# Kernel tuning notes

Hardware: AMD Instinct MI355X
Metric: run time of the kernel (lower is better)

The kernel has to match this reference:

```python
import jax, jax.numpy as jnp
import numpy as np

HIDDEN = 3072
HEADS = 32
HEAD_DIM = HIDDEN // HEADS  # 96


def setup_inputs() -> dict:
    key = jax.random.key(0)
    k1, k2, k3, k4 = jax.random.split(key, 4)
    B, S = 2, 2048
    x = jax.random.normal(k1, (B, S, HIDDEN), dtype=jnp.float32)
    # qkv_proj: Linear(hidden, 3*hidden, bias=False); torch weight is [out,in]
    w_qkv = jax.random.normal(k2, (3 * HIDDEN, HIDDEN), dtype=jnp.float32) * (HIDDEN ** -0.5)
    # o_proj: Linear(hidden, hidden) with bias
    w_o = jax.random.normal(k3, (HIDDEN, HIDDEN), dtype=jnp.float32) * (HIDDEN ** -0.5)
    b_o = jax.random.normal(k4, (HIDDEN,), dtype=jnp.float32) * 0.01
    return {"x": x, "w_qkv": w_qkv, "w_o": w_o, "b_o": b_o}


def reference(x, w_qkv, w_o, b_o):
    B, S, _ = x.shape
    qkv = jnp.einsum('bsh,oh->bso', x, w_qkv)  # [B,S,3*HIDDEN]
    q, k, v = jnp.split(qkv, 3, axis=-1)
    # [B,S,HIDDEN] -> [B,H,S,D]
    def split_heads(t):
        return t.reshape(B, S, HEADS, HEAD_DIM).transpose(0, 2, 1, 3)
    q, k, v = split_heads(q), split_heads(k), split_heads(v)
    scores = jnp.einsum('bhqd,bhkd->bhqk', q, k) / jnp.sqrt(jnp.float32(HEAD_DIM))
    attn = jax.nn.softmax(scores, axis=-1)
    out = jnp.einsum('bhqk,bhkd->bhqd', attn, v)  # [B,H,S,D]
    out = out.transpose(0, 2, 1, 3).reshape(B, S, HIDDEN)
    return jnp.einsum('bsh,oh->bso', out, w_o) + b_o
```

## Files before the change

kernel.cpp:

```cpp
#include <hip/hip_runtime.h>
#include <math.h>


typedef unsigned int u32;
typedef unsigned short u16;
typedef __attribute__((ext_vector_type(8))) short bf16x8;
typedef __attribute__((ext_vector_type(4))) float f32x4;

#define MFMA(a, b, c) __builtin_amdgcn_mfma_f32_16x16x32_bf16((a), (b), (c), 0, 0, 0)

#define GLDS16(g, l) __builtin_amdgcn_global_load_lds( \
    (const __attribute__((address_space(1))) u32*)(g), \
    (__attribute__((address_space(3))) u32*)(l), 16, 0, 0)

__device__ __forceinline__ u16 f2bf(float f) {
  u32 u = __builtin_bit_cast(u32, f);
  return (u16)((u + 0x7fffu + ((u >> 16) & 1u)) >> 16);
}
__device__ __forceinline__ float bf2f(u16 h) {
  u32 u = ((u32)h) << 16;
  return __builtin_bit_cast(float, u);
}
__device__ __forceinline__ void split2(float f, u16& h, u16& l) {
  h = f2bf(f);
  l = f2bf(f - bf2f(h));
}
__device__ __forceinline__ bf16x8 ld16(const u16* p) {
  return *reinterpret_cast<const bf16x8*>(p);
}

__global__ void split_kernel(const float* __restrict__ src, u16* __restrict__ dst,
                             long n) {
  long i = ((long)blockIdx.x * 256 + threadIdx.x) * 4;
  if (i >= n) return;
  const float4 v = *reinterpret_cast<const float4*>(src + i);
  const u32 i32 = (u32)i;
  const u32 row = i32 / 3072u;
  const u32 col = i32 - row * 3072u;
  const long base = (long)row * 6144 + (col >> 5) * 64 + (col & 31);
  ushort4 h, l;
  split2(v.x, h.x, l.x);
  split2(v.y, h.y, l.y);
  split2(v.z, h.z, l.z);
  split2(v.w, h.w, l.w);
  *reinterpret_cast<ushort4*>(dst + base) = h;
  *reinterpret_cast<ushort4*>(dst + base + 32) = l;
}

template <int MODE>
__global__ __launch_bounds__(512, 2) void gemm3t(
    const u16* __restrict__ A2, const u16* __restrict__ B2,
    int M, int N,
    u16* __restrict__ C2, float* __restrict__ Cf, const float* __restrict__ bias) {
  constexpr int NT = 96;
  __shared__ u16 ldsA[2][256 * 64];
  __shared__ u16 ldsB[2][192 * 64];
  const int tid = threadIdx.x;
  const int lane = tid & 63;
  const int w = tid >> 6;
  const int wr = w >> 2, wc = w & 3;
  const int lr = lane & 15, lg = lane >> 4;

  const int mt = M >> 8;
  const int nwg = gridDim.x;
  const int bid = blockIdx.x;
  const int wg = (bid & 7) * (nwg >> 3) + (bid >> 3);
  const int bm = wg % mt, bn = wg / mt;

  const int srow = lane >> 3;
  const int sgc = ((lane & 7) ^ srow) * 8;

  auto stA = [&](int buf, int kt, int j) {
    const int r = j * 64 + w * 8 + srow;
    GLDS16(A2 + (long)(bm * 256 + r) * 6144 + kt * 64 + sgc,
           &ldsA[buf][(j * 64 + w * 8) * 64]);
  };
  auto stB = [&](int buf, int kt, int j) {
    const int r = j * 64 + w * 8 + srow;
    GLDS16(B2 + (long)(bn * 192 + r) * 6144 + kt * 64 + sgc,
           &ldsB[buf][(j * 64 + w * 8) * 64]);
  };

  f32x4 acc[8][3];
#pragma unroll
  for (int m = 0; m < 8; ++m)
#pragma unroll
    for (int n = 0; n < 3; ++n)
#pragma unroll
      for (int j = 0; j < 4; ++j) acc[m][n][j] = 0.f;

  stA(0, 0, 0); stA(0, 0, 1); stA(0, 0, 2); stA(0, 0, 3);
  stB(0, 0, 0); stB(0, 0, 1); stB(0, 0, 2);
  asm volatile("s_waitcnt vmcnt(0)" ::: "memory");
  __builtin_amdgcn_s_barrier();

  const int aRow0 = wr * 128 + lr;
  const int bRow0 = wc * 48 + lr;
  const int c0 = (lg ^ (lr & 7)) * 8;

#define RD_A(MQ)                                                           \
  _Pragma("unroll") for (int m = 0; m < 4; ++m) {                          \
    const int off = (aRow0 + (MQ)*64 + m * 16) * 64 + c0;                  \
    ah[m] = ld16(&LA[off]);                                                \
    al[m] = ld16(&LA[off ^ 32]);                                           \
  }
#define DO_MFMA3(MQ)                                                       \
  __builtin_amdgcn_s_setprio(1);                                           \
  _Pragma("unroll") for (int m = 0; m < 4; ++m)                            \
  _Pragma("unroll") for (int n = 0; n < 3; ++n) {                          \
    acc[(MQ)*4 + m][n] = MFMA(ah[m], bh[n], acc[(MQ)*4 + m][n]);           \
    acc[(MQ)*4 + m][n] = MFMA(ah[m], bl[n], acc[(MQ)*4 + m][n]);           \
    acc[(MQ)*4 + m][n] = MFMA(al[m], bh[n], acc[(MQ)*4 + m][n]);           \
  }                                                                        \
  __builtin_amdgcn_s_setprio(0);
#define PH_SYNC()                                                          \
  __builtin_amdgcn_s_barrier();                                            \
  asm volatile("s_waitcnt lgkmcnt(0)" ::: "memory");                       \
  __builtin_amdgcn_sched_barrier(0);

  for (int t = 0; t < NT; ++t) {
    const int cur = t & 1;
    const int nxt = cur ^ 1;
    const u16* LA = ldsA[cur];
    const u16* LB = ldsB[cur];
    bf16x8 ah[4], al[4], bh[3], bl[3];
#pragma unroll
    for (int n = 0; n < 3; ++n) {
      const int off = (bRow0 + n * 16) * 64 + c0;
      bh[n] = ld16(&LB[off]);
      bl[n] = ld16(&LB[off ^ 32]);
    }
    RD_A(0);
    if (t + 1 < NT) {
      stA(nxt, t + 1, 0); stA(nxt, t + 1, 1);
      stA(nxt, t + 1, 2); stA(nxt, t + 1, 3);
      stB(nxt, t + 1, 0); stB(nxt, t + 1, 1); stB(nxt, t + 1, 2);
    }
    PH_SYNC();
    DO_MFMA3(0);
    __builtin_amdgcn_s_barrier();
    RD_A(1);
    PH_SYNC();
    DO_MFMA3(1);
    asm volatile("s_waitcnt vmcnt(0)" ::: "memory");
    __builtin_amdgcn_s_barrier();
  }
#undef RD_A
#undef DO_MFMA3
#undef PH_SYNC

#pragma unroll
  for (int m = 0; m < 8; ++m)
#pragma unroll
    for (int j = 0; j < 4; ++j) {
      const long row = (long)bm * 256 + wr * 128 + m * 16 + lg * 4 + j;
#pragma unroll
      for (int n = 0; n < 3; ++n) {
        const int col = bn * 192 + wc * 48 + n * 16 + lr;
        const float v = acc[m][n][j];
        if (MODE == 0) {
          const long idx = row * (2L * N) + (col >> 5) * 64 + (col & 31);
          u16 h, l;
          split2(v, h, l);
          C2[idx] = h;
          C2[idx + 32] = l;
        } else {
          Cf[row * N + col] = v + bias[col];
        }
      }
    }
}

__global__ void pack_k(const u16* __restrict__ QKV2, u16* __restrict__ Kp) {
  const int t = blockIdx.x * 256 + threadIdx.x;
  const int lane = t & 63;
  const int rec3 = t >> 6;
  const int c = rec3 % 3;
  const int kb = (rec3 / 3) & 127;
  const int hl = rec3 / 384;
  const int lr = lane & 15, lg = lane >> 4;
  const long src = ((long)((hl >> 5) * 2048 + kb * 16 + lr)) * 18432 +
                   (96 + (hl & 31) * 3 + c) * 64 + lg * 8;
  const long dst = ((long)rec3 * 2) * 512 + lane * 8;
  *reinterpret_cast<bf16x8*>(Kp + dst) = ld16(QKV2 + src);
  *reinterpret_cast<bf16x8*>(Kp + dst + 512) = ld16(QKV2 + src + 32);
}

__global__ __launch_bounds__(256) void pack_v(const u16* __restrict__ QKV2,
                                              u16* __restrict__ Vp) {
  __shared__ u16 sV[2][32 * 96];
  const int tid = threadIdx.x;
  const int hl = blockIdx.x >> 6;
  const int kq = blockIdx.x & 63;
  const long rowbase = ((long)((hl >> 5) * 2048 + kq * 32)) * 18432 +
                       (192 + (hl & 31) * 3) * 64;
#pragma unroll
  for (int i = 0; i < 3; ++i) {
    const int idx = i * 256 + tid;
    const int pl = idx / 384;
    const int r2 = idx % 384;
    const int row = r2 / 12, cu = r2 % 12;
    const long src = rowbase + (long)row * 18432 + (cu >> 2) * 64 + (cu & 3) * 8 + pl * 32;
    *reinterpret_cast<bf16x8*>(&sV[pl][row * 96 + cu * 8]) = ld16(QKV2 + src);
  }
  __syncthreads();
#pragma unroll
  for (int i = 0; i < 3; ++i) {
    const int idx = i * 256 + tid;
    const int lane = idx & 63;
    const int rl = idx >> 6;
    const int n = rl >> 1, pl = rl & 1;
    const int lr = lane & 15, lg = lane >> 4;
    bf16x8 o;
#pragma unroll
    for (int e = 0; e < 8; ++e) o[e] = (short)sV[pl][(lg * 8 + e) * 96 + n * 16 + lr];
    const long dst = ((((long)hl * 6 + n) * 64 + kq) * 2 + pl) * 512 + lane * 8;
    *reinterpret_cast<bf16x8*>(Vp + dst) = o;
  }
}

__global__ __launch_bounds__(256, 2) void attn_kernel(
    const u16* __restrict__ QKV2,
    const u16* __restrict__ Kp, const u16* __restrict__ Vp,
    u16* __restrict__ AO2) {
  __shared__ u16 kv[2][24 * 512];
  __shared__ u16 pb[4][2][512];
  const int lane = threadIdx.x & 63;
  const int wv = threadIdx.x >> 6;
  const int lr = lane & 15, lg = lane >> 4;

  const int nwg = gridDim.x;
  const int bid = blockIdx.x;
  const int wg = (bid & 7) * (nwg >> 3) + (bid >> 3);
  const int hl = wg >> 5;
  const int qblk = wg & 31;
  const int b = hl >> 5;
  const int q0 = qblk * 64 + wv * 16;

  bf16x8 qh[3], ql[3];
  {
    const long qofs =
        ((long)(b * 2048 + q0 + lr)) * 18432 + ((hl & 31) * 3) * 64 + lg * 8;
#pragma unroll
    for (int c = 0; c < 3; ++c) {
      qh[c] = ld16(QKV2 + qofs + c * 64);
      ql[c] = ld16(QKV2 + qofs + c * 64 + 32);
    }
  }

  f32x4 o_acc[6];
#pragma unroll
  for (int n = 0; n < 6; ++n)
#pragma unroll
    for (int j = 0; j < 4; ++j) o_acc[n][j] = 0.f;
  float lsum[4] = {0.f, 0.f, 0.f, 0.f};

  const float scale = 0.10206207261596577f;
  u16* pbh = pb[wv][0];
  u16* pbl = pb[wv][1];

  auto stage = [&](int nb, int it) {
    const long kbase = ((long)hl * 768 + (long)it * 12) * 512;
    const long vbase = ((long)hl * 768 + (long)it * 2) * 512;
#pragma unroll
    for (int j = 0; j < 6; ++j) {
      const int r = wv * 6 + j;
      const u16* src;
      if (r < 12) {
        const int tt = r / 6, rc = r % 6;
        src = Kp + kbase + ((long)(tt * 6 + rc)) * 512 + lane * 8;
      } else {
        const int r2 = r - 12;
        src = Vp + vbase + ((long)((r2 >> 1) * 128 + (r2 & 1))) * 512 + lane * 8;
      }
      GLDS16(src, &kv[nb][r * 512]);
    }
  };

  stage(0, 0);
  __syncthreads();

  for (int it = 0; it < 64; ++it) {
    const int nb = it & 1;
    if (it < 63) stage(nb ^ 1, it + 1);
    const u16* L = kv[nb];

    f32x4 s0, s1;
#pragma unroll
    for (int j = 0; j < 4; ++j) { s0[j] = 0.f; s1[j] = 0.f; }
#pragma unroll
    for (int c = 0; c < 3; ++c) {
      const bf16x8 kh0 = ld16(L + (c * 2 + 0) * 512 + lane * 8);
      const bf16x8 kl0 = ld16(L + (c * 2 + 1) * 512 + lane * 8);
      const bf16x8 kh1 = ld16(L + (6 + c * 2 + 0) * 512 + lane * 8);
      const bf16x8 kl1 = ld16(L + (6 + c * 2 + 1) * 512 + lane * 8);
      s0 = MFMA(qh[c], kh0, s0);
      s1 = MFMA(qh[c], kh1, s1);
      s0 = MFMA(qh[c], kl0, s0);
      s1 = MFMA(qh[c], kl1, s1);
      s0 = MFMA(ql[c], kh0, s0);
      s1 = MFMA(ql[c], kh1, s1);
    }

#pragma unroll
    for (int j = 0; j < 4; ++j) {
      const float p0 = __expf(fmaf(s0[j], scale, -12.f));
      const float p1 = __expf(fmaf(s1[j], scale, -12.f));
      lsum[j] += p0 + p1;
      const int r = lg * 4 + j;
      const int key = j ^ lg;
      u16 h, l;
      split2(p0, h, l);
      const int a0 = r * 32 + ((((lr >> 3) ^ key) & 3) << 3) + (lr & 7);
      pbh[a0] = h;
      pbl[a0] = l;
      split2(p1, h, l);
      const int a1 = r * 32 + ((((2 + (lr >> 3)) ^ key) & 3) << 3) + (lr & 7);
      pbh[a1] = h;
      pbl[a1] = l;
    }
    const int rkey = (lr & 3) ^ (lr >> 2);
    const int ra = lr * 32 + (((lg ^ rkey) & 3) << 3);
    const bf16x8 pah = ld16(&pbh[ra]);
    const bf16x8 pal = ld16(&pbl[ra]);

#pragma unroll
    for (int n = 0; n < 6; ++n) {
      const bf16x8 vh = ld16(L + (12 + n * 2 + 0) * 512 + lane * 8);
      const bf16x8 vl = ld16(L + (12 + n * 2 + 1) * 512 + lane * 8);
      o_acc[n] = MFMA(pah, vh, o_acc[n]);
      o_acc[n] = MFMA(pah, vl, o_acc[n]);
      o_acc[n] = MFMA(pal, vh, o_acc[n]);
    }
    __syncthreads();
  }

  float inv[4];
#pragma unroll
  for (int j = 0; j < 4; ++j) {
    float rs = lsum[j];
#pragma unroll
    for (int mk = 1; mk < 16; mk <<= 1) rs += __shfl_xor(rs, mk);
    inv[j] = 1.f / rs;
  }
#pragma unroll
  for (int n = 0; n < 6; ++n)
#pragma unroll
    for (int j = 0; j < 4; ++j) {
      const long row = (long)(b * 2048 + q0 + lg * 4 + j);
      const long idx =
          row * 6144 + ((hl & 31) * 3 + (n >> 1)) * 64 + (n & 1) * 16 + lr;
      u16 h, l;
      split2(o_acc[n][j] * inv[j], h, l);
      AO2[idx] = h;
      AO2[idx + 32] = l;
    }
}

extern "C" void kernel_launch(void* const* d_in, const int* in_sizes, int n_in,
                              void* d_out, int out_size, void* d_ws, size_t ws_size,
                              hipStream_t stream) {
  const float* x = (const float*)d_in[0];
  const float* wqkv = (const float*)d_in[1];
  const float* wo = (const float*)d_in[2];
  const float* bo = (const float*)d_in[3];
  float* out = (float*)d_out;
  char* ws = (char*)d_ws;

  const size_t E_X = (size_t)4096 * 3072;
  const size_t E_WQ = (size_t)9216 * 3072;
  const size_t E_QKV = (size_t)4096 * 9216;
  const size_t E_WO = (size_t)3072 * 3072;

  u16* X2 = (u16*)ws;
  char* W0 = ws + 4 * E_X;
  u16* W2 = (u16*)W0;
  char* Q0 = W0 + 4 * E_WQ;
  u16* QKV2 = (u16*)Q0;
  char* V0 = Q0 + 4 * E_QKV;
  u16* VP = (u16*)V0;
  u16* KP = (u16*)ws;
  u16* AO2 = (u16*)W0;
  u16* WO2 = (u16*)(W0 + 4 * E_X);

  const size_t need = 4 * (E_X + E_WQ + E_QKV + E_X);
  if (ws_size < need) return;

  split_kernel<<<12288, 256, 0, stream>>>(x, X2, (long)E_X);
  split_kernel<<<27648, 256, 0, stream>>>(wqkv, W2, (long)E_WQ);
  gemm3t<0><<<768, 512, 0, stream>>>(X2, W2, 4096, 9216, QKV2, nullptr, nullptr);
  pack_k<<<6144, 256, 0, stream>>>(QKV2, KP);
  pack_v<<<4096, 256, 0, stream>>>(QKV2, VP);
  split_kernel<<<9216, 256, 0, stream>>>(wo, WO2, (long)E_WO);
  attn_kernel<<<2048, 256, 0, stream>>>(QKV2, KP, VP, AO2);
  gemm3t<1><<<256, 512, 0, stream>>>(AO2, WO2, 4096, 3072, nullptr, out, bo);
}
```

Before: 1.303 ms.

## Halve GEMM workgroup to four waves with larger per-wave tiles

The split-bf16 GEMM drops from 8 waves to 4 waves per 256x192 tile. Each wave now computes a 128x96 sub-tile with 48 accumulators, and the two-phase barrier/setprio pipeline is replaced by a single load-all-then-MFMA loop with __syncthreads. The aim is to raise per-wave register reuse of A/B fragments and cut barrier count. The cost is heavy register pressure (192 accumulator VGPRs plus fragments) and less latency hiding with only 4 waves and one block per CU.

```diff
diff --git a/kernel.cpp b/kernel.cpp
--- a/kernel.cpp
+++ b/kernel.cpp
@@ -48,7 +48,7 @@
 }
 
 template <int MODE>
-__global__ __launch_bounds__(512, 2) void gemm3t(
+__global__ __launch_bounds__(256, 1) void gemm3t(
     const u16* __restrict__ A2, const u16* __restrict__ B2,
     int M, int N,
     u16* __restrict__ C2, float* __restrict__ Cf, const float* __restrict__ bias) {
@@ -58,7 +58,7 @@
   const int tid = threadIdx.x;
   const int lane = tid & 63;
   const int w = tid >> 6;
-  const int wr = w >> 2, wc = w & 3;
+  const int wr = w >> 1, wc = w & 1;
   const int lr = lane & 15, lg = lane >> 4;
 
   const int mt = M >> 8;
@@ -70,84 +70,71 @@
   const int srow = lane >> 3;
   const int sgc = ((lane & 7) ^ srow) * 8;
 
+  const u16* Apan = A2 + (size_t)(bm * 256) * 6144;
+  const u16* Bpan = B2 + (size_t)(bn * 192) * 6144;
+  const u32 laneOff = (u32)((w * 8 + srow) * 6144 + sgc);
+
   auto stA = [&](int buf, int kt, int j) {
-    const int r = j * 64 + w * 8 + srow;
-    GLDS16(A2 + (long)(bm * 256 + r) * 6144 + kt * 64 + sgc,
-           &ldsA[buf][(j * 64 + w * 8) * 64]);
+    GLDS16(Apan + (size_t)kt * 64 + (size_t)j * (32 * 6144) + laneOff,
+           &ldsA[buf][(j * 32 + w * 8) * 64]);
   };
   auto stB = [&](int buf, int kt, int j) {
-    const int r = j * 64 + w * 8 + srow;
-    GLDS16(B2 + (long)(bn * 192 + r) * 6144 + kt * 64 + sgc,
-           &ldsB[buf][(j * 64 + w * 8) * 64]);
+    GLDS16(Bpan + (size_t)kt * 64 + (size_t)j * (32 * 6144) + laneOff,
+           &ldsB[buf][(j * 32 + w * 8) * 64]);
   };
 
-  f32x4 acc[8][3];
+  f32x4 acc[8][6];
 #pragma unroll
   for (int m = 0; m < 8; ++m)
 #pragma unroll
-    for (int n = 0; n < 3; ++n)
+    for (int n = 0; n < 6; ++n)
 #pragma unroll
       for (int j = 0; j < 4; ++j) acc[m][n][j] = 0.f;
 
-  stA(0, 0, 0); stA(0, 0, 1); stA(0, 0, 2); stA(0, 0, 3);
-  stB(0, 0, 0); stB(0, 0, 1); stB(0, 0, 2);
-  asm volatile("s_waitcnt vmcnt(0)" ::: "memory");
-  __builtin_amdgcn_s_barrier();
+#pragma unroll
+  for (int j = 0; j < 8; ++j) stA(0, 0, j);
+#pragma unroll
+  for (int j = 0; j < 6; ++j) stB(0, 0, j);
+  __syncthreads();
 
   const int aRow0 = wr * 128 + lr;
-  const int bRow0 = wc * 48 + lr;
+  const int bRow0 = wc * 96 + lr;
   const int c0 = (lg ^ (lr & 7)) * 8;
-
-#define RD_A(MQ)                                                           \
-  _Pragma("unroll") for (int m = 0; m < 4; ++m) {                          \
-    const int off = (aRow0 + (MQ)*64 + m * 16) * 64 + c0;                  \
-    ah[m] = ld16(&LA[off]);                                                \
-    al[m] = ld16(&LA[off ^ 32]);                                           \
-  }
-#define DO_MFMA3(MQ)                                                       \
-  __builtin_amdgcn_s_setprio(1);                                           \
-  _Pragma("unroll") for (int m = 0; m < 4; ++m)                            \
-  _Pragma("unroll") for (int n = 0; n < 3; ++n) {                          \
-    acc[(MQ)*4 + m][n] = MFMA(ah[m], bh[n], acc[(MQ)*4 + m][n]);           \
-    acc[(MQ)*4 + m][n] = MFMA(ah[m], bl[n], acc[(MQ)*4 + m][n]);           \
-    acc[(MQ)*4 + m][n] = MFMA(al[m], bh[n], acc[(MQ)*4 + m][n]);           \
-  }                                                                        \
-  __builtin_amdgcn_s_setprio(0);
-#define PH_SYNC()                                                          \
-  __builtin_amdgcn_s_barrier();                                            \
-  asm volatile("s_waitcnt lgkmcnt(0)" ::: "memory");                       \
-  __builtin_amdgcn_sched_barrier(0);
 
   for (int t = 0; t < NT; ++t) {
     const int cur = t & 1;
     const int nxt = cur ^ 1;
     const u16* LA = ldsA[cur];
     const u16* LB = ldsB[cur];
-    bf16x8 ah[4], al[4], bh[3], bl[3];
-#pragma unroll
-    for (int n = 0; n < 3; ++n) {
+    if (t + 1 < NT) {
+#pragma unroll
+      for (int j = 0; j < 8; ++j) stA(nxt, t + 1, j);
+#pragma unroll
+      for (int j = 0; j < 6; ++j) stB(nxt, t + 1, j);
+    }
+    __builtin_amdgcn_sched_barrier(0);
+
+    bf16x8 ah[8], al[8];
+#pragma unroll
+    for (int m = 0; m < 8; ++m) {
+      const int off = (aRow0 + m * 16) * 64 + c0;
+      ah[m] = ld16(&LA[off]);
+      al[m] = ld16(&LA[off ^ 32]);
+    }
+#pragma unroll
+    for (int n = 0; n < 6; ++n) {
       const int off = (bRow0 + n * 16) * 64 + c0;
-      bh[n] = ld16(&LB[off]);
-      bl[n] = ld16(&LB[off ^ 32]);
-    }
-    RD_A(0);
-    if (t + 1 < NT) {
-      stA(nxt, t + 1, 0); stA(nxt, t + 1, 1);
-      stA(nxt, t + 1, 2); stA(nxt, t + 1, 3);
-      stB(nxt, t + 1, 0); stB(nxt, t + 1, 1); stB(nxt, t + 1, 2);
-    }
-    PH_SYNC();
-    DO_MFMA3(0);
-    __builtin_amdgcn_s_barrier();
-    RD_A(1);
-    PH_SYNC();
-    DO_MFMA3(1);
-    asm volatile("s_waitcnt vmcnt(0)" ::: "memory");
-    __builtin_amdgcn_s_barrier();
-  }
-#undef RD_A
-#undef DO_MFMA3
-#undef PH_SYNC
+      const bf16x8 bh = ld16(&LB[off]);
+      const bf16x8 bl = ld16(&LB[off ^ 32]);
+#pragma unroll
+      for (int m = 0; m < 8; ++m) {
+        acc[m][n] = MFMA(ah[m], bh, acc[m][n]);
+        acc[m][n] = MFMA(ah[m], bl, acc[m][n]);
+        acc[m][n] = MFMA(al[m], bh, acc[m][n]);
+      }
+    }
+    __syncthreads();
+  }
 
 #pragma unroll
   for (int m = 0; m < 8; ++m)
@@ -155,8 +142,8 @@
     for (int j = 0; j < 4; ++j) {
       const long row = (long)bm * 256 + wr * 128 + m * 16 + lg * 4 + j;
 #pragma unroll
-      for (int n = 0; n < 3; ++n) {
-        const int col = bn * 192 + wc * 48 + n * 16 + lr;
+      for (int n = 0; n < 6; ++n) {
+        const int col = bn * 192 + wc * 96 + n * 16 + lr;
         const float v = acc[m][n][j];
         if (MODE == 0) {
           const long idx = row * (2L * N) + (col >> 5) * 64 + (col & 31);
@@ -388,10 +375,10 @@
 
   split_kernel<<<12288, 256, 0, stream>>>(x, X2, (long)E_X);
   split_kernel<<<27648, 256, 0, stream>>>(wqkv, W2, (long)E_WQ);
-  gemm3t<0><<<768, 512, 0, stream>>>(X2, W2, 4096, 9216, QKV2, nullptr, nullptr);
+  gemm3t<0><<<768, 256, 0, stream>>>(X2, W2, 4096, 9216, QKV2, nullptr, nullptr);
   pack_k<<<6144, 256, 0, stream>>>(QKV2, KP);
   pack_v<<<4096, 256, 0, stream>>>(QKV2, VP);
   split_kernel<<<9216, 256, 0, stream>>>(wo, WO2, (long)E_WO);
   attn_kernel<<<2048, 256, 0, stream>>>(QKV2, KP, VP, AO2);
-  gemm3t<1><<<256, 512, 0, stream>>>(AO2, WO2, 4096, 3072, nullptr, out, bo);
-}
+  gemm3t<1><<<256, 256, 0, stream>>>(AO2, WO2, 4096, 3072, nullptr, out, bo);
+}
```

Result: slower. 1.558 ms (+19.5%).

## Switch split-bf16 GEMM to 32x32x16 MFMA with new warp tiling and swizzle

Applied to the files above, without the earlier changes.

Rewrites the 3-pass split-bf16 GEMM so it uses 32x32x16 MFMA tiles instead of 16x16x32. Each warp now owns a 64x96 sub-tile (2x3 fragments) rather than 128x48, and the LDS swizzle is changed so that fragment reads stay bank-conflict-free. The aim is fewer LDS reads per MFMA and higher MFMA throughput through larger tiles. In exchange it needs a new epilogue index mapping, and the swizzle has to match the load pattern exactly or results will be wrong.

```diff
diff --git a/kernel.cpp b/kernel.cpp
--- a/kernel.cpp
+++ b/kernel.cpp
@@ -6,8 +6,10 @@
 typedef unsigned short u16;
 typedef __attribute__((ext_vector_type(8))) short bf16x8;
 typedef __attribute__((ext_vector_type(4))) float f32x4;
+typedef __attribute__((ext_vector_type(16))) float f32x16;
 
 #define MFMA(a, b, c) __builtin_amdgcn_mfma_f32_16x16x32_bf16((a), (b), (c), 0, 0, 0)
+#define MFMA32(a, b, c) __builtin_amdgcn_mfma_f32_32x32x16_bf16((a), (b), (c), 0, 0, 0)
 
 #define GLDS16(g, l) __builtin_amdgcn_global_load_lds( \
     (const __attribute__((address_space(1))) u32*)(g), \
@@ -48,7 +50,7 @@
 }
 
 template <int MODE>
-__global__ __launch_bounds__(512, 2) void gemm3t(
+__global__ __launch_bounds__(512, 2) void gemm32(
     const u16* __restrict__ A2, const u16* __restrict__ B2,
     int M, int N,
     u16* __restrict__ C2, float* __restrict__ Cf, const float* __restrict__ bias) {
@@ -58,8 +60,9 @@
   const int tid = threadIdx.x;
   const int lane = tid & 63;
   const int w = tid >> 6;
-  const int wr = w >> 2, wc = w & 3;
-  const int lr = lane & 15, lg = lane >> 4;
+  const int wm = w >> 1, wn = w & 1;
+  const int l31 = lane & 31;
+  const int l5 = lane >> 5;
 
   const int mt = M >> 8;
   const int nwg = gridDim.x;
@@ -68,7 +71,7 @@
   const int bm = wg % mt, bn = wg / mt;
 
   const int srow = lane >> 3;
-  const int sgc = ((lane & 7) ^ srow) * 8;
+  const int sgc = ((lane & 7) ^ srow ^ (w & 3)) * 8;
 
   auto stA = [&](int buf, int kt, int j) {
     const int r = j * 64 + w * 8 + srow;
@@ -81,36 +84,41 @@
            &ldsB[buf][(j * 64 + w * 8) * 64]);
   };
 
-  f32x4 acc[8][3];
-#pragma unroll
-  for (int m = 0; m < 8; ++m)
+  f32x16 acc[2][3];
+#pragma unroll
+  for (int m = 0; m < 2; ++m)
 #pragma unroll
     for (int n = 0; n < 3; ++n)
 #pragma unroll
-      for (int j = 0; j < 4; ++j) acc[m][n][j] = 0.f;
+      for (int j = 0; j < 16; ++j) acc[m][n][j] = 0.f;
 
   stA(0, 0, 0); stA(0, 0, 1); stA(0, 0, 2); stA(0, 0, 3);
   stB(0, 0, 0); stB(0, 0, 1); stB(0, 0, 2);
-  asm volatile("s_waitcnt vmcnt(0)" ::: "memory");
-  __builtin_amdgcn_s_barrier();
-
-  const int aRow0 = wr * 128 + lr;
-  const int bRow0 = wc * 48 + lr;
-  const int c0 = (lg ^ (lr & 7)) * 8;
-
-#define RD_A(MQ)                                                           \
-  _Pragma("unroll") for (int m = 0; m < 4; ++m) {                          \
-    const int off = (aRow0 + (MQ)*64 + m * 16) * 64 + c0;                  \
-    ah[m] = ld16(&LA[off]);                                                \
-    al[m] = ld16(&LA[off ^ 32]);                                           \
-  }
-#define DO_MFMA3(MQ)                                                       \
+  __syncthreads();
+
+  const int aRow0 = wm * 64 + l31;
+  const int bRow0 = wn * 96 + l31;
+  const int rk = (lane & 7) ^ ((lane >> 3) & 3);
+
+#define CSLOT(KS, PL) ((((KS)*2 + l5 + (PL)*4) ^ rk) * 8)
+#define RD_PH(KS)                                                          \
+  _Pragma("unroll") for (int n = 0; n < 3; ++n) {                          \
+    const int off = (bRow0 + n * 32) * 64;                                 \
+    b[n][0] = ld16(&LB[off + CSLOT(KS, 0)]);                               \
+    b[n][1] = ld16(&LB[off + CSLOT(KS, 1)]);                               \
+  }                                                                        \
+  _Pragma("unroll") for (int m = 0; m < 2; ++m) {                          \
+    const int off = (aRow0 + m * 32) * 64;                                 \
+    a[m][0] = ld16(&LA[off + CSLOT(KS, 0)]);                               \
+    a[m][1] = ld16(&LA[off + CSLOT(KS, 1)]);                               \
+  }
+#define DO_MFMA3()                                                         \
   __builtin_amdgcn_s_setprio(1);                                           \
-  _Pragma("unroll") for (int m = 0; m < 4; ++m)                            \
+  _Pragma("unroll") for (int m = 0; m < 2; ++m)                            \
   _Pragma("unroll") for (int n = 0; n < 3; ++n) {                          \
-    acc[(MQ)*4 + m][n] = MFMA(ah[m], bh[n], acc[(MQ)*4 + m][n]);           \
-    acc[(MQ)*4 + m][n] = MFMA(ah[m], bl[n], acc[(MQ)*4 + m][n]);           \
-    acc[(MQ)*4 + m][n] = MFMA(al[m], bh[n], acc[(MQ)*4 + m][n]);           \
+    acc[m][n] = MFMA32(a[m][0], b[n][0], acc[m][n]);                       \
+    acc[m][n] = MFMA32(a[m][0], b[n][1], acc[m][n]);                       \
+    acc[m][n] = MFMA32(a[m][1], b[n][0], acc[m][n]);                       \
   }                                                                        \
   __builtin_amdgcn_s_setprio(0);
 #define PH_SYNC()                                                          \
@@ -123,41 +131,37 @@
     const int nxt = cur ^ 1;
     const u16* LA = ldsA[cur];
     const u16* LB = ldsB[cur];
-    bf16x8 ah[4], al[4], bh[3], bl[3];
-#pragma unroll
-    for (int n = 0; n < 3; ++n) {
-      const int off = (bRow0 + n * 16) * 64 + c0;
-      bh[n] = ld16(&LB[off]);
-      bl[n] = ld16(&LB[off ^ 32]);
-    }
-    RD_A(0);
+    bf16x8 a[2][2], b[3][2];
+    RD_PH(0);
     if (t + 1 < NT) {
       stA(nxt, t + 1, 0); stA(nxt, t + 1, 1);
       stA(nxt, t + 1, 2); stA(nxt, t + 1, 3);
       stB(nxt, t + 1, 0); stB(nxt, t + 1, 1); stB(nxt, t + 1, 2);
     }
     PH_SYNC();
-    DO_MFMA3(0);
+    DO_MFMA3();
     __builtin_amdgcn_s_barrier();
-    RD_A(1);
+    RD_PH(1);
     PH_SYNC();
-    DO_MFMA3(1);
+    DO_MFMA3();
     asm volatile("s_waitcnt vmcnt(0)" ::: "memory");
     __builtin_amdgcn_s_barrier();
   }
-#undef RD_A
+#undef CSLOT
+#undef RD_PH
 #undef DO_MFMA3
 #undef PH_SYNC
 
 #pragma unroll
-  for (int m = 0; m < 8; ++m)
-#pragma unroll
-    for (int j = 0; j < 4; ++j) {
-      const long row = (long)bm * 256 + wr * 128 + m * 16 + lg * 4 + j;
-#pragma unroll
-      for (int n = 0; n < 3; ++n) {
-        const int col = bn * 192 + wc * 48 + n * 16 + lr;
-        const float v = acc[m][n][j];
+  for (int mf = 0; mf < 2; ++mf)
+#pragma unroll
+    for (int nf = 0; nf < 3; ++nf) {
+      const int col = bn * 192 + wn * 96 + nf * 32 + l31;
+#pragma unroll
+      for (int reg = 0; reg < 16; ++reg) {
+        const int rif = (reg & 3) + 8 * (reg >> 2) + 4 * l5;
+        const long row = (long)bm * 256 + wm * 64 + mf * 32 + rif;
+        const float v = acc[mf][nf][reg];
         if (MODE == 0) {
           const long idx = row * (2L * N) + (col >> 5) * 64 + (col & 31);
           u16 h, l;
@@ -388,10 +392,10 @@
 
   split_kernel<<<12288, 256, 0, stream>>>(x, X2, (long)E_X);
   split_kernel<<<27648, 256, 0, stream>>>(wqkv, W2, (long)E_WQ);
-  gemm3t<0><<<768, 512, 0, stream>>>(X2, W2, 4096, 9216, QKV2, nullptr, nullptr);
+  gemm32<0><<<768, 512, 0, stream>>>(X2, W2, 4096, 9216, QKV2, nullptr, nullptr);
   pack_k<<<6144, 256, 0, stream>>>(QKV2, KP);
   pack_v<<<4096, 256, 0, stream>>>(QKV2, VP);
   split_kernel<<<9216, 256, 0, stream>>>(wo, WO2, (long)E_WO);
   attn_kernel<<<2048, 256, 0, stream>>>(QKV2, KP, VP, AO2);
-  gemm3t<1><<<256, 512, 0, stream>>>(AO2, WO2, 4096, 3072, nullptr, out, bo);
-}
+  gemm32<1><<<256, 512, 0, stream>>>(AO2, WO2, 4096, 3072, nullptr, out, bo);
+}
```

Result: slower. 1.331 ms (+2.2%).
